# Optimization experiments

Hardware: AMD Instinct MI355X
Metric: run time of the kernel (lower is better)

The kernel has to match this reference:

```python
import jax, jax.numpy as jnp
import numpy as np
import math

DIM = 1024
B, S = 4, 2048

def setup_inputs() -> dict:
    key = jax.random.key(0)
    ks = jax.random.split(key, 4)
    scale = 1.0 / math.sqrt(DIM)
    X = jax.random.normal(ks[0], (B, S, DIM), dtype=jnp.float32)
    W_in = jax.random.normal(ks[1], (3 * DIM, DIM), dtype=jnp.float32) * scale
    b_in = jnp.zeros((3 * DIM,), dtype=jnp.float32)
    W_out = jax.random.normal(ks[2], (DIM, DIM), dtype=jnp.float32) * scale
    b_out = jnp.zeros((DIM,), dtype=jnp.float32)
    attention_mask = jnp.ones((B, 1, S), dtype=jnp.int32)
    return {"X": X, "attention_mask": attention_mask, "W_in": W_in,
            "b_in": b_in, "W_out": W_out, "b_out": b_out}

def reference(X, attention_mask, W_in, b_in, W_out, b_out):
    # in_proj: [B,S,3*DIM]
    qkv = jnp.einsum('bsd,ed->bse', X, W_in) + b_in
    Q, K, V = jnp.split(qkv, 3, axis=-1)
    # scores: [B,S,S]
    scores = jnp.einsum('bqd,bkd->bqk', Q, K)
    # masked_fill happens BEFORE the /sqrt(dim) scaling in the original
    scores = jnp.where(attention_mask == 0, jnp.float32(-1e20), scores)
    attn = jax.nn.softmax(scores / jnp.float32(math.sqrt(DIM)), axis=-1)
    # Dropout(0.1) treated as identity (eval-mode reference)
    out = jnp.einsum('bqk,bkd->bqd', attn, V)
    return jnp.einsum('bsd,od->bso', out, W_out) + b_out
```

## Files before the change

### kernel.cpp

```cpp
#include <hip/hip_runtime.h>
#include <stdint.h>

#define AS1 __attribute__((address_space(1)))
#define AS3 __attribute__((address_space(3)))

typedef __bf16 bf16x8 __attribute__((ext_vector_type(8)));
typedef float f32x4 __attribute__((ext_vector_type(4)));

__device__ __forceinline__ unsigned short f2bf(float f) {
  unsigned u = __float_as_uint(f);
  u += 0x7FFF + ((u >> 16) & 1);
  return (unsigned short)(u >> 16);
}
__device__ __forceinline__ float bf2f(unsigned short h) {
  return __uint_as_float(((unsigned)h) << 16);
}

__global__ __launch_bounds__(256) void cast_kernel(const float* __restrict__ in,
                                                   unsigned short* __restrict__ out,
                                                   int n4) {
  int i = blockIdx.x * 256 + threadIdx.x;
  if (i >= n4) return;
  float4 v = reinterpret_cast<const float4*>(in)[i];
  ushort4 o;
  o.x = f2bf(v.x); o.y = f2bf(v.y); o.z = f2bf(v.z); o.w = f2bf(v.w);
  reinterpret_cast<ushort4*>(out)[i] = o;
}

template<int OUT_BF16>
__global__ __launch_bounds__(256, 2) void gemm_bt(
    const unsigned short* __restrict__ A, long lda, long strideA,
    const unsigned short* __restrict__ B, long ldb, long strideB,
    void* __restrict__ Cv, long ldc, long strideC,
    const float* __restrict__ bias, int K) {
  __shared__ unsigned short sA[128 * 32];
  __shared__ unsigned short sB[128 * 32];
  const int t = threadIdx.x;
  const int lane = t & 63;
  const int wave = t >> 6;

  const unsigned short* Ab = A + (size_t)blockIdx.z * strideA + (size_t)blockIdx.y * 128 * lda;
  const unsigned short* Bb = B + (size_t)blockIdx.z * strideB + (size_t)blockIdx.x * 128 * ldb;

  const int srow = t >> 2;
  const int schunk = (t & 3) * 8;
  const unsigned short* aptr = Ab + (size_t)srow * lda + schunk;
  const unsigned short* bptr = Bb + (size_t)srow * ldb + schunk;
  char* ldsA0 = (char*)&sA[0] + wave * 1024;
  char* ldsB0 = (char*)&sB[0] + wave * 1024;

  f32x4 acc[4][4];
  const f32x4 zero = {0.f, 0.f, 0.f, 0.f};
#pragma unroll
  for (int i = 0; i < 4; i++)
#pragma unroll
    for (int j = 0; j < 4; j++) acc[i][j] = zero;

  const int wm = (wave >> 1) * 64;
  const int wn = (wave & 1) * 64;
  const int fr = lane & 15;
  const int fk = (lane >> 4) * 8;

  for (int k0 = 0; k0 < K; k0 += 32) {
    __syncthreads();
    __builtin_amdgcn_global_load_lds((AS1 void*)(aptr + k0), (AS3 void*)ldsA0, 16, 0, 0);
    __builtin_amdgcn_global_load_lds((AS1 void*)(aptr + 64 * lda + k0), (AS3 void*)(ldsA0 + 4096), 16, 0, 0);
    __builtin_amdgcn_global_load_lds((AS1 void*)(bptr + k0), (AS3 void*)ldsB0, 16, 0, 0);
    __builtin_amdgcn_global_load_lds((AS1 void*)(bptr + 64 * ldb + k0), (AS3 void*)(ldsB0 + 4096), 16, 0, 0);
    __syncthreads();
    bf16x8 af[4], bfv[4];
#pragma unroll
    for (int i = 0; i < 4; i++) {
      af[i]  = *reinterpret_cast<const bf16x8*>(&sA[(wm + i * 16 + fr) * 32 + fk]);
      bfv[i] = *reinterpret_cast<const bf16x8*>(&sB[(wn + i * 16 + fr) * 32 + fk]);
    }
#pragma unroll
    for (int i = 0; i < 4; i++)
#pragma unroll
      for (int j = 0; j < 4; j++)
        acc[i][j] = __builtin_amdgcn_mfma_f32_16x16x32_bf16(af[i], bfv[j], acc[i][j], 0, 0, 0);
  }

  const int quad = lane >> 4;
#pragma unroll
  for (int i = 0; i < 4; i++) {
    int gm = blockIdx.y * 128 + wm + i * 16 + quad * 4;
#pragma unroll
    for (int j = 0; j < 4; j++) {
      int gn = blockIdx.x * 128 + wn + j * 16 + fr;
      float bv = bias ? bias[gn] : 0.0f;
#pragma unroll
      for (int r = 0; r < 4; r++) {
        float val = acc[i][j][r] + bv;
        size_t off = (size_t)blockIdx.z * strideC + (size_t)(gm + r) * ldc + gn;
        if (OUT_BF16)
          ((unsigned short*)Cv)[off] = f2bf(val);
        else
          ((float*)Cv)[off] = val;
      }
    }
  }
}

__global__ __launch_bounds__(256) void transpose_v(const unsigned short* __restrict__ qkv,
                                                   unsigned short* __restrict__ vt) {
  __shared__ unsigned short tile[64][68];
  int t = threadIdx.x;
  int s0 = blockIdx.x * 64, d0 = blockIdx.y * 64, b = blockIdx.z;
  const unsigned short* V = qkv + (size_t)b * 2048 * 3072 + 2048;
  unsigned short* Vt = vt + (size_t)b * 1024 * 2048;
  int r = t >> 4, c = (t & 15) * 4;
#pragma unroll
  for (int i = 0; i < 4; i++) {
    int s = r + i * 16;
    ushort4 v4 = *reinterpret_cast<const ushort4*>(&V[(size_t)(s0 + s) * 3072 + d0 + c]);
    tile[s][c] = v4.x; tile[s][c + 1] = v4.y; tile[s][c + 2] = v4.z; tile[s][c + 3] = v4.w;
  }
  __syncthreads();
#pragma unroll
  for (int i = 0; i < 4; i++) {
    int d = r + i * 16;
    ushort4 o;
    o.x = tile[c][d]; o.y = tile[c + 1][d]; o.z = tile[c + 2][d]; o.w = tile[c + 3][d];
    *reinterpret_cast<ushort4*>(&Vt[(size_t)(d0 + d) * 2048 + s0 + c]) = o;
  }
}

__global__ __launch_bounds__(256) void softmax_kernel(unsigned short* __restrict__ P,
                                                      const int* __restrict__ mask) {
  __shared__ float red[8];
  const int S = 2048;
  int row = blockIdx.x;
  int b = row >> 11;
  unsigned short* prow = P + (size_t)row * S;
  const int* mrow = mask + (size_t)b * S;
  int t = threadIdx.x;
  int base = t * 8;
  uint4 raw = *reinterpret_cast<const uint4*>(&prow[base]);
  int4 m0 = *reinterpret_cast<const int4*>(&mrow[base]);
  int4 m1 = *reinterpret_cast<const int4*>(&mrow[base + 4]);
  unsigned short us[8];
  us[0] = raw.x & 0xffff; us[1] = raw.x >> 16;
  us[2] = raw.y & 0xffff; us[3] = raw.y >> 16;
  us[4] = raw.z & 0xffff; us[5] = raw.z >> 16;
  us[6] = raw.w & 0xffff; us[7] = raw.w >> 16;
  int mk[8] = {m0.x, m0.y, m0.z, m0.w, m1.x, m1.y, m1.z, m1.w};
  float l[8];
  float mx = -3.4e38f;
#pragma unroll
  for (int j = 0; j < 8; j++) {
    float v = bf2f(us[j]);
    v = (mk[j] == 0) ? -1e20f : v;
    l[j] = v * 0.03125f;
    mx = fmaxf(mx, l[j]);
  }
#pragma unroll
  for (int o = 32; o >= 1; o >>= 1) mx = fmaxf(mx, __shfl_xor(mx, o, 64));
  if ((t & 63) == 0) red[t >> 6] = mx;
  __syncthreads();
  mx = fmaxf(fmaxf(red[0], red[1]), fmaxf(red[2], red[3]));
  float e[8], s = 0.f;
#pragma unroll
  for (int j = 0; j < 8; j++) { e[j] = __expf(l[j] - mx); s += e[j]; }
#pragma unroll
  for (int o = 32; o >= 1; o >>= 1) s += __shfl_xor(s, o, 64);
  if ((t & 63) == 0) red[4 + (t >> 6)] = s;
  __syncthreads();
  s = red[4] + red[5] + red[6] + red[7];
  float inv = 1.0f / s;
  unsigned short eo[8];
#pragma unroll
  for (int j = 0; j < 8; j++) eo[j] = f2bf(e[j] * inv);
  uint4 outv;
  outv.x = eo[0] | ((unsigned)eo[1] << 16);
  outv.y = eo[2] | ((unsigned)eo[3] << 16);
  outv.z = eo[4] | ((unsigned)eo[5] << 16);
  outv.w = eo[6] | ((unsigned)eo[7] << 16);
  *reinterpret_cast<uint4*>(&prow[base]) = outv;
}

extern "C" void kernel_launch(void* const* d_in, const int* in_sizes, int n_in,
                              void* d_out, int out_size, void* d_ws, size_t ws_size,
                              hipStream_t stream) {
  const float* X = (const float*)d_in[0];
  const int* mask = (const int*)d_in[1];
  const float* b_in = (const float*)d_in[3];
  const float* W_in = (const float*)d_in[2];
  const float* W_out = (const float*)d_in[4];
  const float* b_out = (const float*)d_in[5];
  float* out = (float*)d_out;

  const int S = 2048, D = 1024;
  char* w = (char*)d_ws;
  unsigned short* Xb  = (unsigned short*)w;
  unsigned short* Wib = (unsigned short*)(w + 16777216);
  unsigned short* Wob = (unsigned short*)(w + 16777216 + 6291456);
  unsigned short* QKV = (unsigned short*)(w + 16777216 + 6291456 + 2097152);
  unsigned short* P   = (unsigned short*)(w + 16777216 + 6291456 + 2097152 + 50331648);
  unsigned short* Vt  = (unsigned short*)(w + 16777216 + 6291456 + 2097152 + 50331648 + 33554432);
  unsigned short* Ob  = Xb;

  cast_kernel<<<8192, 256, 0, stream>>>(X, Xb, 2097152);
  cast_kernel<<<3072, 256, 0, stream>>>(W_in, Wib, 786432);
  cast_kernel<<<1024, 256, 0, stream>>>(W_out, Wob, 262144);

  gemm_bt<1><<<dim3(24, 64, 1), 256, 0, stream>>>(Xb, D, 0, Wib, D, 0,
                                                  QKV, 3 * D, 0, b_in, D);
  transpose_v<<<dim3(32, 16, 4), 256, 0, stream>>>(QKV, Vt);
  gemm_bt<1><<<dim3(16, 16, 4), 256, 0, stream>>>(QKV, 3 * D, (long)S * 3 * D,
                                                  QKV + D, 3 * D, (long)S * 3 * D,
                                                  P, S, (long)S * S, nullptr, D);
  softmax_kernel<<<8192, 256, 0, stream>>>(P, mask);
  gemm_bt<1><<<dim3(8, 16, 4), 256, 0, stream>>>(P, S, (long)S * S,
                                                 Vt, S, (long)D * S,
                                                 Ob, D, (long)S * D, nullptr, S);
  gemm_bt<0><<<dim3(8, 64, 1), 256, 0, stream>>>(Ob, D, 0, Wob, D, 0,
                                                 out, D, 0, b_out, D);
}
```

Measured before the change: 324.6 us.

## Switch GEMM to 32x32x16 MFMA with XOR-swizzled LDS layout

Replaces the 4x4 grid of 16x16x32 bf16 MFMAs per wave with a 2x2 grid of 32x32x16 MFMAs over two k-substeps, halving LDS fragment reads per step. The global-to-LDS load chunk index is XOR-swizzled by row so that fragment reads from LDS avoid bank conflicts. The epilogue is rewritten for the 32x32 accumulator layout. Risks include different register pressure and a less coalesced store pattern in the epilogue.

```diff
diff --git a/kernel.cpp b/kernel.cpp
--- a/kernel.cpp
+++ b/kernel.cpp
@@ -6,6 +6,7 @@
 
 typedef __bf16 bf16x8 __attribute__((ext_vector_type(8)));
 typedef float f32x4 __attribute__((ext_vector_type(4)));
+typedef float f32x16 __attribute__((ext_vector_type(16)));
 
 __device__ __forceinline__ unsigned short f2bf(float f) {
   unsigned u = __float_as_uint(f);
@@ -43,23 +44,34 @@
   const unsigned short* Bb = B + (size_t)blockIdx.z * strideB + (size_t)blockIdx.x * 128 * ldb;
 
   const int srow = t >> 2;
-  const int schunk = (t & 3) * 8;
-  const unsigned short* aptr = Ab + (size_t)srow * lda + schunk;
-  const unsigned short* bptr = Bb + (size_t)srow * ldb + schunk;
+  const int schunk = (t & 3) ^ ((srow >> 1) & 3);
+  const unsigned short* aptr = Ab + (size_t)srow * lda + schunk * 8;
+  const unsigned short* bptr = Bb + (size_t)srow * ldb + schunk * 8;
   char* ldsA0 = (char*)&sA[0] + wave * 1024;
   char* ldsB0 = (char*)&sB[0] + wave * 1024;
 
-  f32x4 acc[4][4];
-  const f32x4 zero = {0.f, 0.f, 0.f, 0.f};
-#pragma unroll
-  for (int i = 0; i < 4; i++)
-#pragma unroll
-    for (int j = 0; j < 4; j++) acc[i][j] = zero;
+  f32x16 acc[2][2];
+#pragma unroll
+  for (int i = 0; i < 2; i++)
+#pragma unroll
+    for (int j = 0; j < 2; j++)
+#pragma unroll
+      for (int r = 0; r < 16; r++) acc[i][j][r] = 0.f;
 
   const int wm = (wave >> 1) * 64;
   const int wn = (wave & 1) * 64;
-  const int fr = lane & 15;
-  const int fk = (lane >> 4) * 8;
+  const int r31 = lane & 31;
+  const int half = lane >> 5;
+  const int swz = (r31 >> 1) & 3;
+
+  int offA[2][2], offB[2][2];
+#pragma unroll
+  for (int i = 0; i < 2; i++)
+#pragma unroll
+    for (int s = 0; s < 2; s++) {
+      offA[i][s] = (wm + i * 32 + r31) * 64 + (((2 * s + half) ^ swz) * 16);
+      offB[i][s] = (wn + i * 32 + r31) * 64 + (((2 * s + half) ^ swz) * 16);
+    }
 
   for (int k0 = 0; k0 < K; k0 += 32) {
     __syncthreads();
@@ -68,31 +80,34 @@
     __builtin_amdgcn_global_load_lds((AS1 void*)(bptr + k0), (AS3 void*)ldsB0, 16, 0, 0);
     __builtin_amdgcn_global_load_lds((AS1 void*)(bptr + 64 * ldb + k0), (AS3 void*)(ldsB0 + 4096), 16, 0, 0);
     __syncthreads();
-    bf16x8 af[4], bfv[4];
-#pragma unroll
-    for (int i = 0; i < 4; i++) {
-      af[i]  = *reinterpret_cast<const bf16x8*>(&sA[(wm + i * 16 + fr) * 32 + fk]);
-      bfv[i] = *reinterpret_cast<const bf16x8*>(&sB[(wn + i * 16 + fr) * 32 + fk]);
+#pragma unroll
+    for (int s = 0; s < 2; s++) {
+      bf16x8 af[2], bfv[2];
+#pragma unroll
+      for (int i = 0; i < 2; i++) {
+        af[i]  = *reinterpret_cast<const bf16x8*>((const char*)sA + offA[i][s]);
+        bfv[i] = *reinterpret_cast<const bf16x8*>((const char*)sB + offB[i][s]);
+      }
+#pragma unroll
+      for (int i = 0; i < 2; i++)
+#pragma unroll
+        for (int j = 0; j < 2; j++)
+          acc[i][j] = __builtin_amdgcn_mfma_f32_32x32x16_bf16(af[i], bfv[j], acc[i][j], 0, 0, 0);
     }
-#pragma unroll
-    for (int i = 0; i < 4; i++)
-#pragma unroll
-      for (int j = 0; j < 4; j++)
-        acc[i][j] = __builtin_amdgcn_mfma_f32_16x16x32_bf16(af[i], bfv[j], acc[i][j], 0, 0, 0);
-  }
-
-  const int quad = lane >> 4;
-#pragma unroll
-  for (int i = 0; i < 4; i++) {
-    int gm = blockIdx.y * 128 + wm + i * 16 + quad * 4;
-#pragma unroll
-    for (int j = 0; j < 4; j++) {
-      int gn = blockIdx.x * 128 + wn + j * 16 + fr;
+  }
+
+#pragma unroll
+  for (int i = 0; i < 2; i++) {
+    int gmb = blockIdx.y * 128 + wm + i * 32;
+#pragma unroll
+    for (int j = 0; j < 2; j++) {
+      int gn = blockIdx.x * 128 + wn + j * 32 + r31;
       float bv = bias ? bias[gn] : 0.0f;
 #pragma unroll
-      for (int r = 0; r < 4; r++) {
+      for (int r = 0; r < 16; r++) {
+        int row = (r & 3) + 8 * (r >> 2) + 4 * half;
         float val = acc[i][j][r] + bv;
-        size_t off = (size_t)blockIdx.z * strideC + (size_t)(gm + r) * ldc + gn;
+        size_t off = (size_t)blockIdx.z * strideC + (size_t)(gmb + row) * ldc + gn;
         if (OUT_BF16)
           ((unsigned short*)Cv)[off] = f2bf(val);
         else
@@ -184,8 +199,8 @@
                               hipStream_t stream) {
   const float* X = (const float*)d_in[0];
   const int* mask = (const int*)d_in[1];
+  const float* W_in = (const float*)d_in[2];
   const float* b_in = (const float*)d_in[3];
-  const float* W_in = (const float*)d_in[2];
   const float* W_out = (const float*)d_in[4];
   const float* b_out = (const float*)d_in[5];
   float* out = (float*)d_out;
```

Result: no change. 327.0 us (+0.7%).
